# Optimization experiments

Hardware: AMD Instinct MI355X
Metric: run time of the kernel (lower is better)

Reference implementation:

```python
import jax, jax.numpy as jnp
import numpy as np

B = 32                 # decode batch (sequences)
NBLK = 128             # blocks per sequence
BLOCK = 16             # tokens per block
H, D = 16, 128         # heads, head_dim
HID = H * D            # 2048
FFN = 8192
VOCAB = 32000
MAXPOS = 8192
KV_LEN = NBLK * BLOCK  # 2048 max context
NUM_BLOCKS = B * NBLK  # 4096
ROPE_THETA = 10000.0


def _rope_cos_sin(pos):
    # pos: [...] int -> cos, sin: [..., D//2]
    inv_freq = 1.0 / (ROPE_THETA ** (jnp.arange(0, D, 2, dtype=jnp.float32) / D))
    ang = pos.astype(jnp.float32)[..., None] * inv_freq
    return jnp.cos(ang), jnp.sin(ang)


def _apply_rope(x, cos, sin):
    # x: [..., D]; cos/sin broadcastable to [..., D//2]; half-split (Llama) rotation
    x1, x2 = jnp.split(x, 2, axis=-1)
    return jnp.concatenate([x1 * cos - x2 * sin, x1 * sin + x2 * cos], axis=-1)


def setup_inputs() -> dict:
    key = jax.random.key(0)
    ks = jax.random.split(key, 12)
    inp = {
        "input_ids": jax.random.randint(ks[0], (B,), 0, VOCAB),
        "positions": jax.random.randint(ks[1], (B,), 0, KV_LEN),
        "kv_cache": jax.random.normal(ks[2], (NUM_BLOCKS, 2, BLOCK, H, D), jnp.float32),
        "block_tables": jnp.arange(NUM_BLOCKS, dtype=jnp.int32).reshape(B, NBLK),
        "context_lens": jax.random.randint(ks[3], (B,), 1, KV_LEN + 1).astype(jnp.int32),
        "embed_tokens": jax.random.normal(ks[4], (VOCAB, HID), jnp.float32) * 0.02,
        "embed_positions": jax.random.normal(ks[5], (MAXPOS, HID), jnp.float32) * 0.02,
        "Wq": jax.random.normal(ks[6], (HID, HID), jnp.float32) / np.float32(np.sqrt(HID)),
        "Wo": jax.random.normal(ks[7], (HID, HID), jnp.float32) / np.float32(np.sqrt(HID)),
        "Wprm": jax.random.normal(ks[8], (HID, HID), jnp.float32) / np.float32(np.sqrt(HID)),
        "W1": jax.random.normal(ks[9], (HID, FFN), jnp.float32) / np.float32(np.sqrt(HID)),
        "W2": jax.random.normal(ks[10], (FFN, HID), jnp.float32) / np.float32(np.sqrt(FFN)),
    }
    return inp


def reference(input_ids, positions, kv_cache, block_tables, context_lens,
              embed_tokens, embed_positions, Wq, Wo, Wprm, W1, W2):
    # token + position embeddings -> [B, HID]
    emb = embed_tokens[input_ids] + embed_positions[positions]

    # query projection with RoPE at the current position (fused RoPE on q)
    q = (emb @ Wq).reshape(B, H, D)
    cos_q, sin_q = _rope_cos_sin(positions)            # [B, D/2]
    q = _apply_rope(q, cos_q[:, None, :], sin_q[:, None, :])

    # paged KV gather: [B, NBLK, 2, BLOCK, H, D]
    kv = kv_cache[block_tables]
    k = kv[:, :, 0].reshape(B, KV_LEN, H, D)
    v = kv[:, :, 1].reshape(B, KV_LEN, H, D)

    # inline RoPE on gathered keys at their cache positions
    tok_pos = jnp.arange(KV_LEN)
    cos_k, sin_k = _rope_cos_sin(tok_pos)              # [S, D/2]
    k = _apply_rope(k, cos_k[None, :, None, :], sin_k[None, :, None, :])

    # decode attention over valid context
    scale = jnp.asarray(D, jnp.float32) ** -0.5
    scores = jnp.einsum("bhd,bshd->bhs", q, k) * scale
    valid = tok_pos[None, :] < context_lens[:, None]   # [B, S]
    scores = jnp.where(valid[:, None, :], scores, jnp.float32(-1e30))
    probs = jax.nn.softmax(scores, axis=-1)
    attn = jnp.einsum("bhs,bshd->bhd", probs, v).reshape(B, HID) @ Wo

    # PRM head + FFN (no activation in source), residual combine
    prm_scores = attn @ Wprm
    ffn_output = (attn @ W1) @ W2
    return ffn_output + prm_scores
```

## Files before the change

### kernel.cpp

```cpp
#include <hip/hip_runtime.h>
#include <hip/hip_bf16.h>
#include <math.h>

#define BATCH   32
#define NBLK    128
#define BLOCK_T 16
#define HEADS   16
#define DHEAD   128
#define HID     2048
#define FFN     8192
#define KV_LEN  2048

#define NSPLIT  16
#define SPLIT_TOKENS 128

__global__ void prep_kernel(const int* __restrict__ ids, const int* __restrict__ pos,
                            const float* __restrict__ et, const float* __restrict__ ep,
                            float* __restrict__ c4f, float* __restrict__ s4f,
                            float* __restrict__ emb) {
    if (blockIdx.x < 512) {
        int s = blockIdx.x * 4 + (threadIdx.x >> 6);
        int i = threadIdx.x & 63;
        float inv = powf(10000.0f, -(float)i / 64.0f);
        float ang = (float)s * inv;
        c4f[s * 64 + i] = cosf(ang);
        s4f[s * 64 + i] = sinf(ang);
    } else {
        int b = blockIdx.x - 512;
        int id = ids[b], p = pos[b];
        const float4* a = (const float4*)(et + (size_t)id * HID);
        const float4* d = (const float4*)(ep + (size_t)p * HID);
        float4* o = (float4*)(emb + (size_t)b * HID);
        for (int c = threadIdx.x; c < HID / 4; c += 256) {
            float4 x = a[c], y = d[c];
            o[c] = make_float4(x.x + y.x, x.y + y.y, x.z + y.z, x.w + y.w);
        }
    }
}

template <int KC>
__device__ __forceinline__ void gemm2_body(
    const float* __restrict__ X, const float* __restrict__ W,
    float* __restrict__ P, int K, int N, int bx, int by, int tid) {
    __shared__ float xs[KC][36];
    const int k0 = by * KC;
    const int j  = bx * 512 + tid * 2;

    #pragma unroll
    for (int t = tid; t < 32 * KC / 4; t += 256) {
        int bb = t / (KC / 4), qq = t % (KC / 4);
        float4 xv = *reinterpret_cast<const float4*>(X + (size_t)bb * K + k0 + 4 * qq);
        xs[4 * qq + 0][bb] = xv.x; xs[4 * qq + 1][bb] = xv.y;
        xs[4 * qq + 2][bb] = xv.z; xs[4 * qq + 3][bb] = xv.w;
    }
    __syncthreads();

    float acc[32][2];
    #pragma unroll
    for (int bb = 0; bb < 32; ++bb) { acc[bb][0] = 0.f; acc[bb][1] = 0.f; }

    const float* wp = W + (size_t)k0 * N + j;
    float2 bufA[16], bufB[16];
    #pragma unroll
    for (int u = 0; u < 16; ++u)
        bufA[u] = *reinterpret_cast<const float2*>(wp + (size_t)u * N);

    #define G2_FMA16(BUF, KK)                                                   \
        _Pragma("unroll")                                                       \
        for (int u = 0; u < 16; ++u) {                                          \
            const float2 w = BUF[u];                                            \
            _Pragma("unroll")                                                   \
            for (int g = 0; g < 8; ++g) {                                       \
                const float4 xv = *reinterpret_cast<const float4*>(&xs[(KK) + u][g * 4]); \
                acc[4*g+0][0] = fmaf(xv.x, w.x, acc[4*g+0][0]);                 \
                acc[4*g+0][1] = fmaf(xv.x, w.y, acc[4*g+0][1]);                 \
                acc[4*g+1][0] = fmaf(xv.y, w.x, acc[4*g+1][0]);                 \
                acc[4*g+1][1] = fmaf(xv.y, w.y, acc[4*g+1][1]);                 \
                acc[4*g+2][0] = fmaf(xv.z, w.x, acc[4*g+2][0]);                 \
                acc[4*g+2][1] = fmaf(xv.z, w.y, acc[4*g+2][1]);                 \
                acc[4*g+3][0] = fmaf(xv.w, w.x, acc[4*g+3][0]);                 \
                acc[4*g+3][1] = fmaf(xv.w, w.y, acc[4*g+3][1]);                 \
            }                                                                   \
        }

    for (int kk = 0; kk < KC; kk += 32) {
        #pragma unroll
        for (int u = 0; u < 16; ++u)
            bufB[u] = *reinterpret_cast<const float2*>(wp + (size_t)(kk + 16 + u) * N);
        G2_FMA16(bufA, kk)
        #pragma unroll
        for (int u = 0; u < 16; ++u) {
            int rr = kk + 32 + u; rr = (rr < KC) ? rr : (KC - 1);
            bufA[u] = *reinterpret_cast<const float2*>(wp + (size_t)rr * N);
        }
        G2_FMA16(bufB, kk + 16)
    }
    #undef G2_FMA16

    float* pp = P + ((size_t)by * 32) * N + j;
    #pragma unroll
    for (int bb = 0; bb < 32; ++bb)
        *reinterpret_cast<float2*>(pp + (size_t)bb * N) = make_float2(acc[bb][0], acc[bb][1]);
}

template <int KC>
__global__ __launch_bounds__(256) void gemm2_kernel(
    const float* __restrict__ X, const float* __restrict__ W,
    float* __restrict__ P, int K, int N) {
    gemm2_body<KC>(X, W, P, K, N, blockIdx.x, blockIdx.y, threadIdx.x);
}

__global__ __launch_bounds__(256) void gemm2_dual_kernel(
    const float* __restrict__ X, const float* __restrict__ Wprm,
    const float* __restrict__ W1,
    float* __restrict__ Pprm, float* __restrict__ P1) {
    if (blockIdx.x < 256) {
        gemm2_body<32>(X, Wprm, Pprm, HID, HID, blockIdx.x & 3, blockIdx.x >> 2, threadIdx.x);
    } else {
        int bb = blockIdx.x - 256;
        gemm2_body<128>(X, W1, P1, HID, FFN, bb & 15, bb >> 4, threadIdx.x);
    }
}

__global__ void red_stage1(const float* __restrict__ PA, const float* __restrict__ PB,
                           int ngA, float* __restrict__ S, int total4) {
    int idx4 = blockIdx.x * 256 + threadIdx.x;
    if (idx4 >= total4) return;
    int g = blockIdx.y;
    const float4* src = (const float4*)((g < ngA) ? PA : PB);
    int c0 = ((g < ngA) ? g : (g - ngA)) * 8;
    float4 s = make_float4(0.f, 0.f, 0.f, 0.f);
    #pragma unroll
    for (int c = 0; c < 8; ++c) {
        float4 v = src[(size_t)(c0 + c) * total4 + idx4];
        s.x += v.x; s.y += v.y; s.z += v.z; s.w += v.w;
    }
    ((float4*)S)[(size_t)g * total4 + idx4] = s;
}

__global__ void red_stage2(const float* __restrict__ S, int ng, int total4,
                           float* __restrict__ out) {
    int idx4 = blockIdx.x * 256 + threadIdx.x;
    if (idx4 >= total4) return;
    float4 s = make_float4(0.f, 0.f, 0.f, 0.f);
    for (int g = 0; g < ng; ++g) {
        float4 v = ((const float4*)S)[(size_t)g * total4 + idx4];
        s.x += v.x; s.y += v.y; s.z += v.z; s.w += v.w;
    }
    ((float4*)out)[idx4] = s;
}

__global__ void reduce4_kernel(const float* __restrict__ P, int nch, int total4,
                               float* __restrict__ out) {
    int idx4 = blockIdx.x * 256 + threadIdx.x;
    if (idx4 >= total4) return;
    const float4* P4 = (const float4*)P;
    float4 s = make_float4(0.f, 0.f, 0.f, 0.f);
    for (int c = 0; c < nch; ++c) {
        float4 v = P4[(size_t)c * total4 + idx4];
        s.x += v.x; s.y += v.y; s.z += v.z; s.w += v.w;
    }
    ((float4*)out)[idx4] = s;
}

__global__ void rope_q_from_S(const float* __restrict__ S, int ng,
                              const int* __restrict__ positions,
                              const float* __restrict__ c4f, const float* __restrict__ s4f,
                              float* __restrict__ qout) {
    int idx = blockIdx.x * 256 + threadIdx.x;
    int i = idx & 63, hh = (idx >> 6) & 15, b = idx >> 10;
    int base = b * HID + hh * DHEAD;
    float q1 = 0.f, q2 = 0.f;
    for (int g = 0; g < ng; ++g) {
        q1 += S[(size_t)g * (BATCH * HID) + base + i];
        q2 += S[(size_t)g * (BATCH * HID) + base + 64 + i];
    }
    int pos = positions[b];
    float co = c4f[pos * 64 + i], si = s4f[pos * 64 + i];
    qout[base + i]      = q1 * co - q2 * si;
    qout[base + 64 + i] = q1 * si + q2 * co;
}

__global__ __launch_bounds__(256) void attn_partial_kernel(
    const float* __restrict__ q, const float* __restrict__ kv,
    const int* __restrict__ block_tables, const int* __restrict__ context_lens,
    const float* __restrict__ c4f, const float* __restrict__ s4f,
    float* __restrict__ pm, float* __restrict__ pl, float* __restrict__ pacc) {
    const int idx = blockIdx.x;
    const int split = idx & (NSPLIT - 1);
    const int h = (idx >> 4) & 15;
    const int b = idx >> 8;
    const int wave = threadIdx.x >> 6, lane = threadIdx.x & 63, l5 = lane & 31;
    const int r = wave * 2 + (lane >> 5);

    const int ctx = context_lens[b];
    const int s_begin = split * SPLIT_TOKENS;
    const int len = min(SPLIT_TOKENS, ctx - s_begin);

    __shared__ int bt[8];
    __shared__ float sm8[8], sl8[8];
    __shared__ float4 sacc[8][32];
    if (threadIdx.x < 8)
        bt[threadIdx.x] = block_tables[b * NBLK + split * 8 + threadIdx.x];
    __syncthreads();

    const float4 qr = *reinterpret_cast<const float4*>(q + b * HID + h * DHEAD + 4 * l5);
    const float sgn2 = (l5 & 16) ? -1.f : 1.f;
    const int fq4 = (l5 & 15) * 4;
    float4 pqs;
    pqs.x = sgn2 * __shfl_xor(qr.x, 16); pqs.y = sgn2 * __shfl_xor(qr.y, 16);
    pqs.z = sgn2 * __shfl_xor(qr.z, 16); pqs.w = sgn2 * __shfl_xor(qr.w, 16);

    float m = -INFINITY, l = 0.f;
    float4 a4 = make_float4(0.f, 0.f, 0.f, 0.f);

    if (len > 0) {
        const int nt = (len + 7) >> 3;
        const int NI = (nt + 3) & ~3;

        #define LOADT(T, K4, V4, C4, S4) {                                         \
            int tc = min((T), len - 1);                                            \
            const float* kp = kv + (size_t)bt[tc >> 4] * 65536                     \
                                 + (size_t)(tc & 15) * 2048 + h * DHEAD;           \
            K4 = *reinterpret_cast<const float4*>(kp + 4 * l5);                    \
            V4 = *reinterpret_cast<const float4*>(kp + 32768 + 4 * l5);            \
            C4 = *reinterpret_cast<const float4*>(c4f + (size_t)(s_begin + tc) * 64 + fq4); \
            S4 = *reinterpret_cast<const float4*>(s4f + (size_t)(s_begin + tc) * 64 + fq4); \
        }

        #define PROCT(T, K4, V4, C4, S4) {                                         \
            float cfx = fmaf(pqs.x, S4.x, qr.x * C4.x);                            \
            float cfy = fmaf(pqs.y, S4.y, qr.y * C4.y);                            \
            float cfz = fmaf(pqs.z, S4.z, qr.z * C4.z);                            \
            float cfw = fmaf(pqs.w, S4.w, qr.w * C4.w);                            \
            float dot = fmaf(K4.x, cfx, fmaf(K4.y, cfy, fmaf(K4.z, cfz, K4.w * cfw))); \
            dot += __shfl_xor(dot, 1);  dot += __shfl_xor(dot, 2);                 \
            dot += __shfl_xor(dot, 4);  dot += __shfl_xor(dot, 8);                 \
            dot += __shfl_xor(dot, 16);                                            \
            float d = ((T) < len) ? dot * 0.08838834764831845f : -INFINITY;        \
            float mn = fmaxf(m, d);                                                \
            float ms = fmaxf(mn, -3.0e38f);                                        \
            float corr = __expf(m - ms);                                           \
            float e = __expf(d - ms);                                              \
            l = l * corr + e;                                                      \
            a4.x = fmaf(e, V4.x, a4.x * corr);                                     \
            a4.y = fmaf(e, V4.y, a4.y * corr);                                     \
            a4.z = fmaf(e, V4.z, a4.z * corr);                                     \
            a4.w = fmaf(e, V4.w, a4.w * corr);                                     \
            m = mn;                                                                \
        }

        float4 kA, vA, cA, sA, kB, vB, cB, sB;
        float4 kC, vC, cC, sC, kD, vD, cD, sD;
        LOADT(r,      kA, vA, cA, sA);
        LOADT(r + 8,  kB, vB, cB, sB);
        LOADT(r + 16, kC, vC, cC, sC);
        LOADT(r + 24, kD, vD, cD, sD);

        for (int i = 0; i < NI; i += 4) {
            int t = r + 8 * i;
            PROCT(t,      kA, vA, cA, sA);  LOADT(t + 32, kA, vA, cA, sA);
            PROCT(t + 8,  kB, vB, cB, sB);  LOADT(t + 40, kB, vB, cB, sB);
            PROCT(t + 16, kC, vC, cC, sC);  LOADT(t + 48, kC, vC, cC, sC);
            PROCT(t + 24, kD, vD, cD, sD);  LOADT(t + 56, kD, vD, cD, sD);
        }
        #undef LOADT
        #undef PROCT
    }

    if (l5 == 0) { sm8[r] = m; sl8[r] = l; }
    sacc[r][l5] = a4;
    __syncthreads();

    if (threadIdx.x < 32) {
        float M = -INFINITY;
        #pragma unroll
        for (int rr = 0; rr < 8; ++rr) M = fmaxf(M, sm8[rr]);
        float L = 0.f;
        float4 o = make_float4(0.f, 0.f, 0.f, 0.f);
        #pragma unroll
        for (int rr = 0; rr < 8; ++rr) {
            float ew = (sm8[rr] == -INFINITY) ? 0.f : __expf(sm8[rr] - M);
            L += sl8[rr] * ew;
            float4 v = sacc[rr][threadIdx.x];
            o.x = fmaf(v.x, ew, o.x); o.y = fmaf(v.y, ew, o.y);
            o.z = fmaf(v.z, ew, o.z); o.w = fmaf(v.w, ew, o.w);
        }
        if (threadIdx.x == 0) { pm[idx] = M; pl[idx] = L; }
        *reinterpret_cast<float4*>(pacc + (size_t)idx * 128 + 4 * threadIdx.x) = o;
    }
}

__global__ void attn_combine_kernel(const float* __restrict__ pm, const float* __restrict__ pl,
                                    const float* __restrict__ pacc, float* __restrict__ attn_out) {
    const int bh = blockIdx.x;
    const int l5 = threadIdx.x;
    if (l5 >= 32) return;
    const int base = bh * NSPLIT;
    float M = -INFINITY;
    #pragma unroll
    for (int sp = 0; sp < NSPLIT; ++sp) M = fmaxf(M, pm[base + sp]);
    float L = 0.f;
    float4 o = make_float4(0.f, 0.f, 0.f, 0.f);
    #pragma unroll
    for (int sp = 0; sp < NSPLIT; ++sp) {
        float mv = pm[base + sp];
        float ew = (mv == -INFINITY) ? 0.f : __expf(mv - M);
        L += pl[base + sp] * ew;
        float4 v = *reinterpret_cast<const float4*>(pacc + (size_t)(base + sp) * 128 + 4 * l5);
        o.x = fmaf(v.x, ew, o.x); o.y = fmaf(v.y, ew, o.y);
        o.z = fmaf(v.z, ew, o.z); o.w = fmaf(v.w, ew, o.w);
    }
    float inv = 1.f / L;
    *reinterpret_cast<float4*>(attn_out + bh * 128 + 4 * l5) =
        make_float4(o.x * inv, o.y * inv, o.z * inv, o.w * inv);
}

extern "C" void kernel_launch(void* const* d_in, const int* in_sizes, int n_in,
                              void* d_out, int out_size, void* d_ws, size_t ws_size,
                              hipStream_t stream) {
    const int*   input_ids    = (const int*)d_in[0];
    const int*   positions    = (const int*)d_in[1];
    const float* kv_cache     = (const float*)d_in[2];
    const int*   block_tables = (const int*)d_in[3];
    const int*   context_lens = (const int*)d_in[4];
    const float* embed_tokens = (const float*)d_in[5];
    const float* embed_pos    = (const float*)d_in[6];
    const float* Wq  = (const float*)d_in[7];
    const float* Wo  = (const float*)d_in[8];
    const float* Wprm= (const float*)d_in[9];
    const float* W1  = (const float*)d_in[10];
    const float* W2  = (const float*)d_in[11];
    float* out = (float*)d_out;

    char* ws = (char*)d_ws;
    size_t off = 0;
    float* c4f  = (float*)(ws + off); off += (size_t)KV_LEN * 64 * 4;
    float* s4f  = (float*)(ws + off); off += (size_t)KV_LEN * 64 * 4;
    float* emb  = (float*)(ws + off); off += (size_t)BATCH * HID * 4;
    float* qbuf = (float*)(ws + off); off += (size_t)BATCH * HID * 4;
    float* attn = (float*)(ws + off); off += (size_t)BATCH * HID * 4;
    float* ao   = (float*)(ws + off); off += (size_t)BATCH * HID * 4;
    float* h1   = (float*)(ws + off); off += (size_t)BATCH * FFN * 4;
    float* pm   = (float*)(ws + off); off += (size_t)BATCH * HEADS * NSPLIT * 4;
    float* plv  = (float*)(ws + off); off += (size_t)BATCH * HEADS * NSPLIT * 4;
    float* pacc = (float*)(ws + off); off += (size_t)BATCH * HEADS * NSPLIT * 128 * 4;
    float* S    = (float*)(ws + off); off += (size_t)16 * BATCH * HID * 4;
    float* P    = (float*)(ws + off); off += (size_t)64 * BATCH * FFN * 4;
    float* Pprm = (float*)(ws + off); off += (size_t)64 * BATCH * HID * 4;
    (void)ws_size; (void)in_sizes; (void)n_in; (void)out_size;

    const int T4_HID = BATCH * HID / 4;
    const int T4_FFN = BATCH * FFN / 4;

    prep_kernel<<<544, 256, 0, stream>>>(input_ids, positions, embed_tokens, embed_pos,
                                         c4f, s4f, emb);
    gemm2_kernel<32><<<dim3(4, 64), 256, 0, stream>>>(emb, Wq, P, HID, HID);
    red_stage1<<<dim3(64, 8), 256, 0, stream>>>(P, P, 8, S, T4_HID);
    rope_q_from_S<<<128, 256, 0, stream>>>(S, 8, positions, c4f, s4f, qbuf);
    attn_partial_kernel<<<BATCH * HEADS * NSPLIT, 256, 0, stream>>>(
        qbuf, kv_cache, block_tables, context_lens, c4f, s4f, pm, plv, pacc);
    attn_combine_kernel<<<BATCH * HEADS, 64, 0, stream>>>(pm, plv, pacc, attn);
    gemm2_kernel<32><<<dim3(4, 64), 256, 0, stream>>>(attn, Wo, P, HID, HID);
    red_stage1<<<dim3(64, 8), 256, 0, stream>>>(P, P, 8, S, T4_HID);
    red_stage2<<<64, 256, 0, stream>>>(S, 8, T4_HID, ao);
    gemm2_dual_kernel<<<512, 256, 0, stream>>>(ao, Wprm, W1, Pprm, P);
    reduce4_kernel<<<256, 256, 0, stream>>>(P, 16, T4_FFN, h1);
    gemm2_kernel<128><<<dim3(4, 64), 256, 0, stream>>>(h1, W2, P, FFN, HID);
    red_stage1<<<dim3(64, 16), 256, 0, stream>>>(P, Pprm, 8, S, T4_HID);
    red_stage2<<<64, 256, 0, stream>>>(S, 16, T4_HID, out);
}
```

Before: 301.4 us.

## Register-prefetch shared X rows in GEMM inner loop and split dual kernel

Restructures the split-K GEMM inner loop so each shared-memory row of X is loaded into registers one step ahead (double-buffered xA/xB) while FMAs run on the previous row. Weight prefetch depth drops from 16 to 8 rows per buffer to make room. It also removes the fused dual kernel and launches the PRM and W1 GEMMs as two separate kernels. P1 gets its own workspace buffer, and P is shrunk to the HID size. The intent is to hide LDS latency, at the cost of higher register pressure, a shallower global prefetch, and one extra launch.

```diff
diff --git a/kernel.cpp b/kernel.cpp
--- a/kernel.cpp
+++ b/kernel.cpp
@@ -60,42 +60,66 @@
     for (int bb = 0; bb < 32; ++bb) { acc[bb][0] = 0.f; acc[bb][1] = 0.f; }
 
     const float* wp = W + (size_t)k0 * N + j;
-    float2 bufA[16], bufB[16];
-    #pragma unroll
-    for (int u = 0; u < 16; ++u)
-        bufA[u] = *reinterpret_cast<const float2*>(wp + (size_t)u * N);
-
-    #define G2_FMA16(BUF, KK)                                                   \
-        _Pragma("unroll")                                                       \
-        for (int u = 0; u < 16; ++u) {                                          \
-            const float2 w = BUF[u];                                            \
-            _Pragma("unroll")                                                   \
-            for (int g = 0; g < 8; ++g) {                                       \
-                const float4 xv = *reinterpret_cast<const float4*>(&xs[(KK) + u][g * 4]); \
-                acc[4*g+0][0] = fmaf(xv.x, w.x, acc[4*g+0][0]);                 \
-                acc[4*g+0][1] = fmaf(xv.x, w.y, acc[4*g+0][1]);                 \
-                acc[4*g+1][0] = fmaf(xv.y, w.x, acc[4*g+1][0]);                 \
-                acc[4*g+1][1] = fmaf(xv.y, w.y, acc[4*g+1][1]);                 \
-                acc[4*g+2][0] = fmaf(xv.z, w.x, acc[4*g+2][0]);                 \
-                acc[4*g+2][1] = fmaf(xv.z, w.y, acc[4*g+2][1]);                 \
-                acc[4*g+3][0] = fmaf(xv.w, w.x, acc[4*g+3][0]);                 \
-                acc[4*g+3][1] = fmaf(xv.w, w.y, acc[4*g+3][1]);                 \
-            }                                                                   \
-        }
-
-    for (int kk = 0; kk < KC; kk += 32) {
+    float2 wA[8], wB[8];
+    float4 xA[8], xB[8];
+    #pragma unroll
+    for (int u = 0; u < 8; ++u)
+        wA[u] = *reinterpret_cast<const float2*>(wp + (size_t)u * N);
+    #pragma unroll
+    for (int g = 0; g < 8; ++g)
+        xA[g] = *reinterpret_cast<const float4*>(&xs[0][g * 4]);
+
+    #define ROW_FMA(XC, XN, WREG, ROWN)                                        \
+    {                                                                          \
+        XN[0] = *reinterpret_cast<const float4*>(&xs[ROWN][0]);                \
+        XN[1] = *reinterpret_cast<const float4*>(&xs[ROWN][4]);                \
+        XN[2] = *reinterpret_cast<const float4*>(&xs[ROWN][8]);                \
+        XN[3] = *reinterpret_cast<const float4*>(&xs[ROWN][12]);               \
+        XN[4] = *reinterpret_cast<const float4*>(&xs[ROWN][16]);               \
+        XN[5] = *reinterpret_cast<const float4*>(&xs[ROWN][20]);               \
+        XN[6] = *reinterpret_cast<const float4*>(&xs[ROWN][24]);               \
+        XN[7] = *reinterpret_cast<const float4*>(&xs[ROWN][28]);               \
+        const float2 w = WREG;                                                 \
+        _Pragma("unroll")                                                      \
+        for (int g = 0; g < 8; ++g) {                                          \
+            acc[4*g+0][0] = fmaf(XC[g].x, w.x, acc[4*g+0][0]);                 \
+            acc[4*g+0][1] = fmaf(XC[g].x, w.y, acc[4*g+0][1]);                 \
+            acc[4*g+1][0] = fmaf(XC[g].y, w.x, acc[4*g+1][0]);                 \
+            acc[4*g+1][1] = fmaf(XC[g].y, w.y, acc[4*g+1][1]);                 \
+            acc[4*g+2][0] = fmaf(XC[g].z, w.x, acc[4*g+2][0]);                 \
+            acc[4*g+2][1] = fmaf(XC[g].z, w.y, acc[4*g+2][1]);                 \
+            acc[4*g+3][0] = fmaf(XC[g].w, w.x, acc[4*g+3][0]);                 \
+            acc[4*g+3][1] = fmaf(XC[g].w, w.y, acc[4*g+3][1]);                 \
+        }                                                                      \
+    }
+
+    for (int kk = 0; kk < KC; kk += 16) {
         #pragma unroll
-        for (int u = 0; u < 16; ++u)
-            bufB[u] = *reinterpret_cast<const float2*>(wp + (size_t)(kk + 16 + u) * N);
-        G2_FMA16(bufA, kk)
+        for (int u = 0; u < 8; ++u)
+            wB[u] = *reinterpret_cast<const float2*>(wp + (size_t)(kk + 8 + u) * N);
+        ROW_FMA(xA, xB, wA[0], kk + 1)
+        ROW_FMA(xB, xA, wA[1], kk + 2)
+        ROW_FMA(xA, xB, wA[2], kk + 3)
+        ROW_FMA(xB, xA, wA[3], kk + 4)
+        ROW_FMA(xA, xB, wA[4], kk + 5)
+        ROW_FMA(xB, xA, wA[5], kk + 6)
+        ROW_FMA(xA, xB, wA[6], kk + 7)
+        ROW_FMA(xB, xA, wA[7], kk + 8)
         #pragma unroll
-        for (int u = 0; u < 16; ++u) {
-            int rr = kk + 32 + u; rr = (rr < KC) ? rr : (KC - 1);
-            bufA[u] = *reinterpret_cast<const float2*>(wp + (size_t)rr * N);
-        }
-        G2_FMA16(bufB, kk + 16)
-    }
-    #undef G2_FMA16
+        for (int u = 0; u < 8; ++u) {
+            int rr = kk + 16 + u; rr = (rr < KC) ? rr : (KC - 1);
+            wA[u] = *reinterpret_cast<const float2*>(wp + (size_t)rr * N);
+        }
+        ROW_FMA(xA, xB, wB[0], kk + 9)
+        ROW_FMA(xB, xA, wB[1], kk + 10)
+        ROW_FMA(xA, xB, wB[2], kk + 11)
+        ROW_FMA(xB, xA, wB[3], kk + 12)
+        ROW_FMA(xA, xB, wB[4], kk + 13)
+        ROW_FMA(xB, xA, wB[5], kk + 14)
+        ROW_FMA(xA, xB, wB[6], kk + 15)
+        ROW_FMA(xB, xA, wB[7], ((kk + 16 < KC) ? (kk + 16) : (KC - 1)))
+    }
+    #undef ROW_FMA
 
     float* pp = P + ((size_t)by * 32) * N + j;
     #pragma unroll
@@ -108,18 +132,6 @@
     const float* __restrict__ X, const float* __restrict__ W,
     float* __restrict__ P, int K, int N) {
     gemm2_body<KC>(X, W, P, K, N, blockIdx.x, blockIdx.y, threadIdx.x);
-}
-
-__global__ __launch_bounds__(256) void gemm2_dual_kernel(
-    const float* __restrict__ X, const float* __restrict__ Wprm,
-    const float* __restrict__ W1,
-    float* __restrict__ Pprm, float* __restrict__ P1) {
-    if (blockIdx.x < 256) {
-        gemm2_body<32>(X, Wprm, Pprm, HID, HID, blockIdx.x & 3, blockIdx.x >> 2, threadIdx.x);
-    } else {
-        int bb = blockIdx.x - 256;
-        gemm2_body<128>(X, W1, P1, HID, FFN, bb & 15, bb >> 4, threadIdx.x);
-    }
 }
 
 __global__ void red_stage1(const float* __restrict__ PA, const float* __restrict__ PB,
@@ -346,7 +358,8 @@
     float* plv  = (float*)(ws + off); off += (size_t)BATCH * HEADS * NSPLIT * 4;
     float* pacc = (float*)(ws + off); off += (size_t)BATCH * HEADS * NSPLIT * 128 * 4;
     float* S    = (float*)(ws + off); off += (size_t)16 * BATCH * HID * 4;
-    float* P    = (float*)(ws + off); off += (size_t)64 * BATCH * FFN * 4;
+    float* P    = (float*)(ws + off); off += (size_t)64 * BATCH * HID * 4;
+    float* P1   = (float*)(ws + off); off += (size_t)16 * BATCH * FFN * 4;
     float* Pprm = (float*)(ws + off); off += (size_t)64 * BATCH * HID * 4;
     (void)ws_size; (void)in_sizes; (void)n_in; (void)out_size;
 
@@ -364,8 +377,9 @@
     gemm2_kernel<32><<<dim3(4, 64), 256, 0, stream>>>(attn, Wo, P, HID, HID);
     red_stage1<<<dim3(64, 8), 256, 0, stream>>>(P, P, 8, S, T4_HID);
     red_stage2<<<64, 256, 0, stream>>>(S, 8, T4_HID, ao);
-    gemm2_dual_kernel<<<512, 256, 0, stream>>>(ao, Wprm, W1, Pprm, P);
-    reduce4_kernel<<<256, 256, 0, stream>>>(P, 16, T4_FFN, h1);
+    gemm2_kernel<32><<<dim3(4, 64), 256, 0, stream>>>(ao, Wprm, Pprm, HID, HID);
+    gemm2_kernel<128><<<dim3(16, 16), 256, 0, stream>>>(ao, W1, P1, HID, FFN);
+    reduce4_kernel<<<256, 256, 0, stream>>>(P1, 16, T4_FFN, h1);
     gemm2_kernel<128><<<dim3(4, 64), 256, 0, stream>>>(h1, W2, P, FFN, HID);
     red_stage1<<<dim3(64, 16), 256, 0, stream>>>(P, Pprm, 8, S, T4_HID);
     red_stage2<<<64, 256, 0, stream>>>(S, 16, T4_HID, out);
```

Measured after the change: 323.3 us. 7.3% more time.

## Remap attention partials so each block covers all heads over one 32-token chunk

Applied to the files above, without the earlier changes.

The attention partial kernel now launches one 512-thread block per (batch, 32-token chunk), with each half-wave handling one head and walking tokens sequentially. A warp therefore reads whole contiguous token rows of K/V across all heads, and the shared-memory intra-block combine and syncthreads are removed. The trade-off is four times as many partial results (64 splits instead of 16), which makes the combine kernel's loop longer. Each half-wave also runs a serial token chain with fewer independent rows in flight to hide latency.

```diff
diff --git a/kernel.cpp b/kernel.cpp
--- a/kernel.cpp
+++ b/kernel.cpp
@@ -11,8 +11,8 @@
 #define FFN     8192
 #define KV_LEN  2048
 
-#define NSPLIT  16
-#define SPLIT_TOKENS 128
+#define NSPLIT2 64
+#define TOKSPL  32
 
 __global__ void prep_kernel(const int* __restrict__ ids, const int* __restrict__ pos,
                             const float* __restrict__ et, const float* __restrict__ ep,
@@ -181,28 +181,26 @@
     qout[base + 64 + i] = q1 * si + q2 * co;
 }
 
-__global__ __launch_bounds__(256) void attn_partial_kernel(
+__global__ __launch_bounds__(512) void attn_partial_kernel(
     const float* __restrict__ q, const float* __restrict__ kv,
     const int* __restrict__ block_tables, const int* __restrict__ context_lens,
     const float* __restrict__ c4f, const float* __restrict__ s4f,
     float* __restrict__ pm, float* __restrict__ pl, float* __restrict__ pacc) {
     const int idx = blockIdx.x;
-    const int split = idx & (NSPLIT - 1);
-    const int h = (idx >> 4) & 15;
-    const int b = idx >> 8;
-    const int wave = threadIdx.x >> 6, lane = threadIdx.x & 63, l5 = lane & 31;
-    const int r = wave * 2 + (lane >> 5);
+    const int split = idx & (NSPLIT2 - 1);
+    const int b = idx >> 6;
+    const int tid = threadIdx.x;
+    const int h = tid >> 5;
+    const int l5 = tid & 31;
 
     const int ctx = context_lens[b];
-    const int s_begin = split * SPLIT_TOKENS;
-    const int len = min(SPLIT_TOKENS, ctx - s_begin);
-
-    __shared__ int bt[8];
-    __shared__ float sm8[8], sl8[8];
-    __shared__ float4 sacc[8][32];
-    if (threadIdx.x < 8)
-        bt[threadIdx.x] = block_tables[b * NBLK + split * 8 + threadIdx.x];
-    __syncthreads();
+    const int s_begin = split * TOKSPL;
+    const int len = min(TOKSPL, ctx - s_begin);
+
+    const int bt0 = block_tables[b * NBLK + split * 2];
+    const int bt1 = block_tables[b * NBLK + split * 2 + 1];
+
+    const int out_idx = (b * HEADS + h) * NSPLIT2 + split;
 
     const float4 qr = *reinterpret_cast<const float4*>(q + b * HID + h * DHEAD + 4 * l5);
     const float sgn2 = (l5 & 16) ? -1.f : 1.f;
@@ -215,12 +213,12 @@
     float4 a4 = make_float4(0.f, 0.f, 0.f, 0.f);
 
     if (len > 0) {
-        const int nt = (len + 7) >> 3;
-        const int NI = (nt + 3) & ~3;
+        const int NI = (len + 3) & ~3;
 
         #define LOADT(T, K4, V4, C4, S4) {                                         \
             int tc = min((T), len - 1);                                            \
-            const float* kp = kv + (size_t)bt[tc >> 4] * 65536                     \
+            int blk = (tc & 16) ? bt1 : bt0;                                       \
+            const float* kp = kv + (size_t)blk * 65536                             \
                                  + (size_t)(tc & 15) * 2048 + h * DHEAD;           \
             K4 = *reinterpret_cast<const float4*>(kp + 4 * l5);                    \
             V4 = *reinterpret_cast<const float4*>(kp + 32768 + 4 * l5);            \
@@ -252,43 +250,23 @@
 
         float4 kA, vA, cA, sA, kB, vB, cB, sB;
         float4 kC, vC, cC, sC, kD, vD, cD, sD;
-        LOADT(r,      kA, vA, cA, sA);
-        LOADT(r + 8,  kB, vB, cB, sB);
-        LOADT(r + 16, kC, vC, cC, sC);
-        LOADT(r + 24, kD, vD, cD, sD);
-
-        for (int i = 0; i < NI; i += 4) {
-            int t = r + 8 * i;
-            PROCT(t,      kA, vA, cA, sA);  LOADT(t + 32, kA, vA, cA, sA);
-            PROCT(t + 8,  kB, vB, cB, sB);  LOADT(t + 40, kB, vB, cB, sB);
-            PROCT(t + 16, kC, vC, cC, sC);  LOADT(t + 48, kC, vC, cC, sC);
-            PROCT(t + 24, kD, vD, cD, sD);  LOADT(t + 56, kD, vD, cD, sD);
+        LOADT(0, kA, vA, cA, sA);
+        LOADT(1, kB, vB, cB, sB);
+        LOADT(2, kC, vC, cC, sC);
+        LOADT(3, kD, vD, cD, sD);
+
+        for (int t = 0; t < NI; t += 4) {
+            PROCT(t,     kA, vA, cA, sA);  LOADT(t + 4, kA, vA, cA, sA);
+            PROCT(t + 1, kB, vB, cB, sB);  LOADT(t + 5, kB, vB, cB, sB);
+            PROCT(t + 2, kC, vC, cC, sC);  LOADT(t + 6, kC, vC, cC, sC);
+            PROCT(t + 3, kD, vD, cD, sD);  LOADT(t + 7, kD, vD, cD, sD);
         }
         #undef LOADT
         #undef PROCT
     }
 
-    if (l5 == 0) { sm8[r] = m; sl8[r] = l; }
-    sacc[r][l5] = a4;
-    __syncthreads();
-
-    if (threadIdx.x < 32) {
-        float M = -INFINITY;
-        #pragma unroll
-        for (int rr = 0; rr < 8; ++rr) M = fmaxf(M, sm8[rr]);
-        float L = 0.f;
-        float4 o = make_float4(0.f, 0.f, 0.f, 0.f);
-        #pragma unroll
-        for (int rr = 0; rr < 8; ++rr) {
-            float ew = (sm8[rr] == -INFINITY) ? 0.f : __expf(sm8[rr] - M);
-            L += sl8[rr] * ew;
-            float4 v = sacc[rr][threadIdx.x];
-            o.x = fmaf(v.x, ew, o.x); o.y = fmaf(v.y, ew, o.y);
-            o.z = fmaf(v.z, ew, o.z); o.w = fmaf(v.w, ew, o.w);
-        }
-        if (threadIdx.x == 0) { pm[idx] = M; pl[idx] = L; }
-        *reinterpret_cast<float4*>(pacc + (size_t)idx * 128 + 4 * threadIdx.x) = o;
-    }
+    if (l5 == 0) { pm[out_idx] = m; pl[out_idx] = l; }
+    *reinterpret_cast<float4*>(pacc + (size_t)out_idx * 128 + 4 * l5) = a4;
 }
 
 __global__ void attn_combine_kernel(const float* __restrict__ pm, const float* __restrict__ pl,
@@ -296,14 +274,12 @@
     const int bh = blockIdx.x;
     const int l5 = threadIdx.x;
     if (l5 >= 32) return;
-    const int base = bh * NSPLIT;
+    const int base = bh * NSPLIT2;
     float M = -INFINITY;
-    #pragma unroll
-    for (int sp = 0; sp < NSPLIT; ++sp) M = fmaxf(M, pm[base + sp]);
+    for (int sp = 0; sp < NSPLIT2; ++sp) M = fmaxf(M, pm[base + sp]);
     float L = 0.f;
     float4 o = make_float4(0.f, 0.f, 0.f, 0.f);
-    #pragma unroll
-    for (int sp = 0; sp < NSPLIT; ++sp) {
+    for (int sp = 0; sp < NSPLIT2; ++sp) {
         float mv = pm[base + sp];
         float ew = (mv == -INFINITY) ? 0.f : __expf(mv - M);
         L += pl[base + sp] * ew;
@@ -342,9 +318,9 @@
     float* attn = (float*)(ws + off); off += (size_t)BATCH * HID * 4;
     float* ao   = (float*)(ws + off); off += (size_t)BATCH * HID * 4;
     float* h1   = (float*)(ws + off); off += (size_t)BATCH * FFN * 4;
-    float* pm   = (float*)(ws + off); off += (size_t)BATCH * HEADS * NSPLIT * 4;
-    float* plv  = (float*)(ws + off); off += (size_t)BATCH * HEADS * NSPLIT * 4;
-    float* pacc = (float*)(ws + off); off += (size_t)BATCH * HEADS * NSPLIT * 128 * 4;
+    float* pm   = (float*)(ws + off); off += (size_t)BATCH * HEADS * NSPLIT2 * 4;
+    float* plv  = (float*)(ws + off); off += (size_t)BATCH * HEADS * NSPLIT2 * 4;
+    float* pacc = (float*)(ws + off); off += (size_t)BATCH * HEADS * NSPLIT2 * 128 * 4;
     float* S    = (float*)(ws + off); off += (size_t)16 * BATCH * HID * 4;
     float* P    = (float*)(ws + off); off += (size_t)64 * BATCH * FFN * 4;
     float* Pprm = (float*)(ws + off); off += (size_t)64 * BATCH * HID * 4;
@@ -358,7 +334,7 @@
     gemm2_kernel<32><<<dim3(4, 64), 256, 0, stream>>>(emb, Wq, P, HID, HID);
     red_stage1<<<dim3(64, 8), 256, 0, stream>>>(P, P, 8, S, T4_HID);
     rope_q_from_S<<<128, 256, 0, stream>>>(S, 8, positions, c4f, s4f, qbuf);
-    attn_partial_kernel<<<BATCH * HEADS * NSPLIT, 256, 0, stream>>>(
+    attn_partial_kernel<<<BATCH * NSPLIT2, 512, 0, stream>>>(
         qbuf, kv_cache, block_tables, context_lens, c4f, s4f, pm, plv, pacc);
     attn_combine_kernel<<<BATCH * HEADS, 64, 0, stream>>>(pm, plv, pacc, attn);
     gemm2_kernel<32><<<dim3(4, 64), 256, 0, stream>>>(attn, Wo, P, HID, HID);
```

Result: faster. 285.4 us (-5.3%).
